# Optimization experiments

Measured on AMD Instinct MI355X. Metric: run time of the kernel, lower is better.

The kernel has to match this reference:

```python
import jax, jax.numpy as jnp
import numpy as np

B_SI = 4.1491   # neutron scattering length Si (fm)
B_O = 5.803     # neutron scattering length O (fm)
CUTOFF = 3.5    # tetrahedral neighbour cutoff (A)
BIG = 1e6       # masked-distance sentinel (finite to keep grads NaN-free)


def setup_inputs() -> dict:
    key = jax.random.key(0)
    k1, k2 = jax.random.split(key)
    N, L = 4096, 40.0
    positions = jax.random.uniform(k1, (N, 3), dtype=jnp.float32) * L
    cell = (L * jnp.eye(3)).astype(jnp.float32)
    r_bins = (0.05 + 0.05 * jnp.arange(200, dtype=jnp.float32))      # 0.05..10.0 A
    q_bins = jnp.linspace(0.5, 25.0, 500, dtype=jnp.float32)          # A^-1
    species = jax.random.randint(k2, (N,), 0, 3, dtype=jnp.int32)     # 0=Si, 1/2=O
    return {"positions": positions, "cell": cell, "r_bins": r_bins,
            "q_bins": q_bins, "species": species}


def _pair_geometry(positions, cell):
    # Minimum-image displacements under a general periodic cell.
    disp = positions[:, None, :] - positions[None, :, :]        # [N,N,3]
    frac = disp @ jnp.linalg.inv(cell)
    frac = frac - jnp.round(frac)
    disp = frac @ cell
    d2 = jnp.sum(disp * disp, axis=-1)                           # [N,N]
    self_mask = jnp.eye(positions.shape[0], dtype=bool)
    dist = jnp.sqrt(jnp.where(self_mask, 1.0, d2))               # safe sqrt on diag
    return disp, dist, self_mask


def reference(positions, cell, r_bins, q_bins, species):
    N = positions.shape[0]
    nbins = r_bins.shape[0]
    dtype = positions.dtype

    disp, dist, self_mask = _pair_geometry(positions, cell)

    # --- neutron-weighted G(r): differentiable linear (cloud-in-cell) binning ---
    b = jnp.where(species == 0, B_SI, B_O).astype(dtype)         # per-atom scattering length
    w = (b[:, None] * b[None, :]) / (jnp.mean(b) ** 2)           # Faber-Ziman pair weights
    r0, dr = r_bins[0], r_bins[1] - r_bins[0]
    x = (dist - r0) / dr
    i0 = jnp.floor(x).astype(jnp.int32)
    f = x - i0.astype(dtype)
    valid = (~self_mask) & (i0 >= 0) & (i0 < nbins - 1)
    w0 = jnp.where(valid, w * (1.0 - f), 0.0).ravel()
    w1 = jnp.where(valid, w * f, 0.0).ravel()
    i0f = jnp.clip(i0, 0, nbins - 1).ravel()
    hist = (jnp.zeros(nbins, dtype)
            .at[i0f].add(w0)
            .at[jnp.clip(i0f + 1, 0, nbins - 1)].add(w1))
    V = jnp.abs(jnp.linalg.det(cell))
    rho = N / V
    shell = 4.0 * jnp.pi * r_bins ** 2 * dr                       # ideal-gas shell volume
    G_r = hist / (N * rho * shell)                                # [nbins]

    # --- total correlation function T(r) = 4 pi rho r G(r) ---
    T_r = 4.0 * jnp.pi * rho * r_bins * G_r

    # --- structure factor S(Q) = 1 + 4 pi rho int r^2 (G(r)-1) sinc(Qr) dr ---
    qr = q_bins[:, None] * r_bins[None, :]                        # [nQ, nr]
    integrand = (r_bins ** 2) * (G_r - 1.0)
    S_Q = 1.0 + 4.0 * jnp.pi * rho * dr * jnp.sum(
        integrand[None, :] * jnp.sinc(qr / jnp.pi), axis=1)

    # --- tetrahedral order parameter q_tet over Si centres with O neighbours ---
    central = species == 0
    nbr_ok = (species != 0)[None, :] & (~self_mask)
    nd = jnp.where(nbr_ok, dist, BIG)
    negd, idx = jax.lax.top_k(-nd, 4)                             # 4 nearest O per atom
    d4 = -negd                                                    # [N,4]
    u = jnp.take_along_axis(disp, idx[:, :, None], axis=1) / d4[:, :, None]  # unit vecs
    cosang = jnp.einsum('nkd,nld->nkl', u, u)                     # [N,4,4]
    pair_mask = jnp.triu(jnp.ones((4, 4), bool), 1)               # 6 angle pairs
    q_i = 1.0 - (3.0 / 8.0) * jnp.sum(((cosang + 1.0 / 3.0) ** 2) * pair_mask, axis=(1, 2))
    vf = (central & (d4[:, 3] < CUTOFF)).astype(dtype)            # needs 4 nbrs in cutoff
    q_tet = jnp.sum(q_i * vf) / jnp.maximum(jnp.sum(vf), 1.0)

    return G_r, T_r, S_Q, q_tet
```

## Files before the change

### kernel.cpp

```cpp
#include <hip/hip_runtime.h>
#include <climits>
#include <math.h>


#define B_SI_F 4.1491f
#define B_O_F  5.803f
#define CUTOFF_F 3.5f
#define CS2 12.25350025f
#define NCOPIES 16
#define CAP 32

#define WS_HIST 16
#define WS_ACC  3328
#define WS_CNT  4096

__device__ __forceinline__ bool dless(float da, int ia, float db, int ib) {
    return (da < db) || (da == db && ia < ib);
}

struct CellK {
    float ci0, ci1, ci2, ci3, ci4, ci5, ci6, ci7, ci8;
    float c0, c1, c2, c3, c4, c5, c6, c7, c8;
};

__device__ __forceinline__ CellK make_cell(const float* __restrict__ cellm,
                                           bool& diag) {
    CellK K;
    K.c0 = cellm[0]; K.c1 = cellm[1]; K.c2 = cellm[2];
    K.c3 = cellm[3]; K.c4 = cellm[4]; K.c5 = cellm[5];
    K.c6 = cellm[6]; K.c7 = cellm[7]; K.c8 = cellm[8];
    double m0 = K.c0, m1 = K.c1, m2 = K.c2;
    double m3 = K.c3, m4 = K.c4, m5 = K.c5;
    double m6 = K.c6, m7 = K.c7, m8 = K.c8;
    double det = m0*(m4*m8 - m5*m7) - m1*(m3*m8 - m5*m6) + m2*(m3*m7 - m4*m6);
    double rd = 1.0 / det;
    K.ci0 = (float)( (m4*m8 - m5*m7) * rd);
    K.ci1 = (float)(-(m1*m8 - m2*m7) * rd);
    K.ci2 = (float)( (m1*m5 - m2*m4) * rd);
    K.ci3 = (float)(-(m3*m8 - m5*m6) * rd);
    K.ci4 = (float)( (m0*m8 - m2*m6) * rd);
    K.ci5 = (float)(-(m0*m5 - m2*m3) * rd);
    K.ci6 = (float)( (m3*m7 - m4*m6) * rd);
    K.ci7 = (float)(-(m0*m7 - m1*m6) * rd);
    K.ci8 = (float)( (m0*m4 - m1*m3) * rd);
    diag = (K.c1 == 0.0f) && (K.c2 == 0.0f) && (K.c3 == 0.0f) &&
           (K.c5 == 0.0f) && (K.c6 == 0.0f) && (K.c7 == 0.0f);
    return K;
}

template<bool DIAG>
__device__ __forceinline__ void min_image(const CellK& K,
                                          float dx, float dy, float dz,
                                          float& ex, float& ey, float& ez) {
    if (DIAG) {
        float t0 = dx * K.ci0, t1 = dy * K.ci4, t2 = dz * K.ci8;
        t0 -= rintf(t0);  t1 -= rintf(t1);  t2 -= rintf(t2);
        ex = t0 * K.c0;  ey = t1 * K.c4;  ez = t2 * K.c8;
    } else {
        float f0 = dx*K.ci0 + dy*K.ci3 + dz*K.ci6;
        float f1 = dx*K.ci1 + dy*K.ci4 + dz*K.ci7;
        float f2 = dx*K.ci2 + dy*K.ci5 + dz*K.ci8;
        f0 -= rintf(f0);  f1 -= rintf(f1);  f2 -= rintf(f2);
        ex = f0*K.c0 + f1*K.c3 + f2*K.c6;
        ey = f0*K.c1 + f1*K.c4 + f2*K.c7;
        ez = f0*K.c2 + f1*K.c5 + f2*K.c8;
    }
}

template<bool DIAG>
__device__ __forceinline__ void hist_sweep(const CellK& K,
                                           const float4* __restrict__ sj,
                                           const float4* __restrict__ sjc,
                                           int lbase, int jb0,
                                           float fi0, float fi1, float fi2,
                                           float xi, float yi, float zi,
                                           float wi, float inv_dr, float nrb0,
                                           float dmax2, int nbins_m1,
                                           float* shist,
                                           bool iSi, bool iO, bool offdiag, int iidx,
                                           float* __restrict__ cnt,
                                           float4* __restrict__ cand) {
    #pragma unroll 4
    for (int l = 0; l < 32; ++l) {
        const float4 pj = sj[lbase + l];
        float d0 = fi0 - pj.x;  d0 -= rintf(d0);
        float d1 = fi1 - pj.y;  d1 -= rintf(d1);
        float d2 = fi2 - pj.z;  d2 -= rintf(d2);
        float ex, ey, ez;
        if (DIAG) {
            ex = d0 * K.c0;  ey = d1 * K.c4;  ez = d2 * K.c8;
        } else {
            ex = d0*K.c0 + d1*K.c3 + d2*K.c6;
            ey = d0*K.c1 + d1*K.c4 + d2*K.c7;
            ez = d0*K.c2 + d1*K.c5 + d2*K.c8;
        }
        float dsq = fmaf(ex, ex, fmaf(ey, ey, ez * ez));
        if (dsq < dmax2) {
            float dist = __builtin_amdgcn_sqrtf(dsq);
            float x  = fmaf(dist, inv_dr, nrb0);
            float fl = floorf(x);
            int   i0 = (int)fl;
            if ((unsigned)i0 < (unsigned)nbins_m1) {
                float w  = wi * pj.w;
                float wf = w * (x - fl);
                atomicAdd(&shist[i0],     w - wf);
                atomicAdd(&shist[i0 + 1], wf);
            }
            if (dsq < CS2) {
                const int jg = jb0 + lbase + l;
                if (iSi && pj.w == B_O_F) {
                    float old = atomicAdd(&cnt[iidx], 1.0f);
                    int slot = (int)rintf(old);
                    if (slot < CAP) {
                        float4 cj = sjc[lbase + l];
                        cj.w = __int_as_float(jg);
                        cand[iidx * CAP + slot] = cj;
                    }
                }
                if (offdiag && iO && pj.w == B_SI_F) {
                    float old = atomicAdd(&cnt[jg], 1.0f);
                    int slot = (int)rintf(old);
                    if (slot < CAP)
                        cand[jg * CAP + slot] = make_float4(xi, yi, zi, __int_as_float(iidx));
                }
            }
        }
    }
}

__global__ __launch_bounds__(256) void k_main(const float* __restrict__ cellm,
                                              const float* __restrict__ pos,
                                              const int* __restrict__ species,
                                              const float* __restrict__ rbins,
                                              float* __restrict__ ws,
                                              int N, int nbins, int T) {
    const int tid = threadIdx.x;
    const int bid = blockIdx.x;

    bool diag;
    const CellK K = make_cell(cellm, diag);

    __shared__ float shist[256];
    __shared__ float sjf[64 * 4];
    __shared__ float sjc[64 * 4];
    shist[tid] = 0.0f;

    const int jhalf = bid & 1;
    int rem = bid >> 1, ti = 0;
    while (rem >= T - ti) { rem -= T - ti; ti++; }
    const int tj  = ti + rem;
    const int jb0 = tj * 128 + jhalf * 64;

    if (tid < 192) {
        int g = 3 * jb0 + tid;
        sjc[(tid / 3) * 4 + (tid % 3)] = (g < 3 * N) ? pos[g] : 0.0f;
    } else {
        int a = tid - 192;
        int ja = jb0 + a;
        sjf[a * 4 + 3] = (ja < N) ? ((species[ja] == 0) ? B_SI_F : B_O_F) : 0.0f;
    }
    __syncthreads();
    if (tid < 64) {
        float x = sjc[tid*4], y = sjc[tid*4+1], z = sjc[tid*4+2];
        float f0, f1, f2;
        if (diag) { f0 = x*K.ci0; f1 = y*K.ci4; f2 = z*K.ci8; }
        else {
            f0 = x*K.ci0 + y*K.ci3 + z*K.ci6;
            f1 = x*K.ci1 + y*K.ci4 + z*K.ci7;
            f2 = x*K.ci2 + y*K.ci5 + z*K.ci8;
        }
        sjf[tid*4] = f0;  sjf[tid*4+1] = f1;  sjf[tid*4+2] = f2;
    }

    const float rb0      = rbins[0];
    const float dr       = rbins[1] - rbins[0];
    const float inv_dr   = 1.0f / dr;
    const float nrb0     = -rb0 * inv_dr;
    const int   nbins_m1 = nbins - 1;
    const float dmax     = fmaf((float)nbins_m1, dr, rb0);
    const float dmax2    = dmax * dmax * 1.000001f;

    const int il  = tid & 127;
    const int sub = tid >> 7;
    const int i   = ti * 128 + il;
    const int ig  = min(i, N - 1);
    const float xi = pos[3*ig], yi = pos[3*ig+1], zi = pos[3*ig+2];
    float fi0, fi1, fi2;
    if (diag) { fi0 = xi*K.ci0; fi1 = yi*K.ci4; fi2 = zi*K.ci8; }
    else {
        fi0 = xi*K.ci0 + yi*K.ci3 + zi*K.ci6;
        fi1 = xi*K.ci1 + yi*K.ci4 + zi*K.ci7;
        fi2 = xi*K.ci2 + yi*K.ci5 + zi*K.ci8;
    }
    const int   spi  = species[ig];
    const float b_i  = (spi == 0) ? B_SI_F : B_O_F;
    const float wmul = (ti == tj) ? 1.0f : 2.0f;
    const float wi   = (i < N) ? b_i * wmul : 0.0f;
    const bool iSi = (i < N) && (spi == 0);
    const bool iO  = (i < N) && (spi != 0);
    const bool offdiag = (ti != tj);

    float*  cnt  = ws + WS_CNT;
    float4* cand = (float4*)(ws + WS_CNT + (size_t)N);

    __syncthreads();

    const float4* sj   = (const float4*)sjf;
    const float4* sjc4 = (const float4*)sjc;
    const int lbase = sub * 32;
    if (diag) hist_sweep<true >(K, sj, sjc4, lbase, jb0, fi0, fi1, fi2, xi, yi, zi, wi, inv_dr, nrb0, dmax2, nbins_m1, shist, iSi, iO, offdiag, i, cnt, cand);
    else      hist_sweep<false>(K, sj, sjc4, lbase, jb0, fi0, fi1, fi2, xi, yi, zi, wi, inv_dr, nrb0, dmax2, nbins_m1, shist, iSi, iO, offdiag, i, cnt, cand);

    __syncthreads();

    float* gh = ws + WS_HIST + (size_t)(bid % NCOPIES) * nbins;
    for (int t = tid; t < nbins; t += 256) {
        float h = shist[t];
        if (h != 0.0f) atomicAdd(&gh[t], h);
    }
}

#define INS4D(c, jc, ex, ey, ez)                                           \
{                                                                          \
    if (dless(c, jc, e3, j3)) {                                            \
        bool lt2 = dless(c, jc, e2, j2);                                   \
        bool lt1 = dless(c, jc, e1, j1);                                   \
        bool lt0 = dless(c, jc, e0, j0);                                   \
        e3 = lt2 ? e2 : c;               j3 = lt2 ? j2 : jc;               \
        x3 = lt2 ? x2 : ex;  y3 = lt2 ? y2 : ey;  z3 = lt2 ? z2 : ez;      \
        e2 = lt2 ? (lt1 ? e1 : c) : e2;  j2 = lt2 ? (lt1 ? j1 : jc) : j2;  \
        x2 = lt2 ? (lt1 ? x1 : ex) : x2;                                   \
        y2 = lt2 ? (lt1 ? y1 : ey) : y2;                                   \
        z2 = lt2 ? (lt1 ? z1 : ez) : z2;                                   \
        e1 = lt1 ? (lt0 ? e0 : c) : e1;  j1 = lt1 ? (lt0 ? j0 : jc) : j1;  \
        x1 = lt1 ? (lt0 ? x0 : ex) : x1;                                   \
        y1 = lt1 ? (lt0 ? y0 : ey) : y1;                                   \
        z1 = lt1 ? (lt0 ? z0 : ez) : z1;                                   \
        e0 = lt0 ? c : e0;               j0 = lt0 ? jc : j0;               \
        x0 = lt0 ? ex : x0;  y0 = lt0 ? ey : y0;  z0 = lt0 ? ez : z0;      \
    }                                                                      \
}

__device__ __forceinline__ float fast_sinc(float x) {
    float rev = x * 0.15915494309189535f;
    rev -= rintf(rev);
    float sn = __builtin_amdgcn_sinf(rev);
    return sn * __builtin_amdgcn_rcpf(x);
}

__global__ __launch_bounds__(256) void k_fin(const float* __restrict__ cellm,
                                             float* __restrict__ ws,
                                             const float* __restrict__ rbins,
                                             const float* __restrict__ qbins,
                                             const int* __restrict__ species,
                                             const float* __restrict__ pos,
                                             float* __restrict__ out,
                                             int N, int nbins, int nq,
                                             int QB, int BT) {
    const int tid = threadIdx.x;
    const int bid = blockIdx.x;

    if (bid >= QB) {
        __shared__ float swq[4], swv[4];
        __shared__ float sacc[128];
        __shared__ int   slast;
        const int tb   = bid - QB;
        const int wid  = tid >> 6;
        const int lane = tid & 63;
        const int s = __builtin_amdgcn_readfirstlane(tb * 4 + wid);

        float* cnt = ws + WS_CNT;
        const float4* cand = (const float4*)(ws + WS_CNT + (size_t)N);

        float qiv = 0.0f, vf = 0.0f;
        if (s < N && species[s] == 0) {
            bool diag;
            const CellK K = make_cell(cellm, diag);
            const float xi = pos[3*s], yi = pos[3*s+1], zi = pos[3*s+2];
            const int c = (int)rintf(cnt[s]);
            if (lane == 0) cnt[s] = 0.0f;

            float e0 = 1e30f, e1 = 1e30f, e2 = 1e30f, e3 = 1e30f;
            int   j0 = INT_MAX, j1 = INT_MAX, j2 = INT_MAX, j3 = INT_MAX;
            float x0 = 0, y0 = 0, z0 = 0, x1 = 0, y1 = 0, z1 = 0;
            float x2 = 0, y2 = 0, z2 = 0, x3 = 0, y3 = 0, z3 = 0;

            if (c <= CAP) {
                if (lane < c) {
                    float4 cd = cand[s * CAP + lane];
                    int j = __float_as_int(cd.w);
                    float ex, ey, ez;
                    if (diag) min_image<true >(K, xi - cd.x, yi - cd.y, zi - cd.z, ex, ey, ez);
                    else      min_image<false>(K, xi - cd.x, yi - cd.y, zi - cd.z, ex, ey, ez);
                    e0 = fmaf(ex, ex, fmaf(ey, ey, ez * ez));
                    j0 = j;  x0 = ex;  y0 = ey;  z0 = ez;
                }
            } else {
                for (int k = lane; k < N; k += 64) {
                    int   sp = species[k];
                    float px = pos[3*k], py = pos[3*k+1], pz = pos[3*k+2];
                    float ex, ey, ez;
                    if (diag) min_image<true >(K, xi - px, yi - py, zi - pz, ex, ey, ez);
                    else      min_image<false>(K, xi - px, yi - py, zi - pz, ex, ey, ez);
                    float d2 = fmaf(ex, ex, fmaf(ey, ey, ez * ez));
                    float cc = (sp != 0 && k != s) ? d2 : 1e30f;
                    int   jc = k;
                    INS4D(cc, jc, ex, ey, ez)
                }
            }

            float r0d, r1d, r2d, r3d;
            int   r0j, r1j, r2j, r3j;
            float rx[4], ry[4], rz[4];
            #define EXTRACT_MIN(RD, RJ, RK)                                    \
            {                                                                  \
                float md = e0; int mj = j0;                                    \
                float mx = x0, my = y0, mz = z0;                               \
                for (int off = 32; off > 0; off >>= 1) {                       \
                    float od = __shfl_xor(md, off, 64);                        \
                    int   oj = __shfl_xor(mj, off, 64);                        \
                    float ox = __shfl_xor(mx, off, 64);                        \
                    float oy = __shfl_xor(my, off, 64);                        \
                    float oz = __shfl_xor(mz, off, 64);                        \
                    bool keep = dless(md, mj, od, oj);                         \
                    md = keep ? md : od;  mj = keep ? mj : oj;                 \
                    mx = keep ? mx : ox;  my = keep ? my : oy;                 \
                    mz = keep ? mz : oz;                                       \
                }                                                              \
                RD = md; RJ = mj; rx[RK] = mx; ry[RK] = my; rz[RK] = mz;       \
                bool pop = (j0 == mj);                                         \
                e0 = pop ? e1 : e0;  j0 = pop ? j1 : j0;                       \
                x0 = pop ? x1 : x0;  y0 = pop ? y1 : y0;  z0 = pop ? z1 : z0;  \
                e1 = pop ? e2 : e1;  j1 = pop ? j2 : j1;                       \
                x1 = pop ? x2 : x1;  y1 = pop ? y2 : y1;  z1 = pop ? z2 : z1;  \
                e2 = pop ? e3 : e2;  j2 = pop ? j3 : j2;                       \
                x2 = pop ? x3 : x2;  y2 = pop ? y3 : y2;  z2 = pop ? z3 : z2;  \
                e3 = pop ? 1e30f : e3;  j3 = pop ? INT_MAX : j3;               \
            }
            EXTRACT_MIN(r0d, r0j, 0)
            EXTRACT_MIN(r1d, r1j, 1)
            EXTRACT_MIN(r2d, r2j, 2)
            EXTRACT_MIN(r3d, r3j, 3)
            #undef EXTRACT_MIN

            if (lane == 0 && r3j != INT_MAX) {
                float dd[4] = {sqrtf(r0d), sqrtf(r1d), sqrtf(r2d), sqrtf(r3d)};
                if (dd[3] < CUTOFF_F) {
                    float ux[4], uy[4], uz[4];
                    #pragma unroll
                    for (int k = 0; k < 4; ++k) {
                        ux[k] = rx[k] / dd[k];
                        uy[k] = ry[k] / dd[k];
                        uz[k] = rz[k] / dd[k];
                    }
                    float s2 = 0.0f;
                    #pragma unroll
                    for (int k = 0; k < 4; ++k)
                        #pragma unroll
                        for (int l = k + 1; l < 4; ++l) {
                            float cs = ux[k]*ux[l] + uy[k]*uy[l] + uz[k]*uz[l];
                            float t  = cs + (1.0f / 3.0f);
                            s2 += t * t;
                        }
                    qiv = 1.0f - 0.375f * s2;
                    vf  = 1.0f;
                }
            }
        }
        if (lane == 0) { swq[wid] = qiv; swv[wid] = vf; }
        __syncthreads();
        if (tid == 0) {
            float bsq = swq[0] + swq[1] + swq[2] + swq[3];
            float bsv = swv[0] + swv[1] + swv[2] + swv[3];
            atomicAdd(&ws[WS_ACC + (tb & 63)], bsq);
            atomicAdd(&ws[WS_ACC + 64 + (tb & 63)], bsv);
            asm volatile("s_waitcnt vmcnt(0)" ::: "memory");
            float old = atomicAdd(&ws[WS_ACC + 128], 1.0f);
            slast = (old > (float)BT - 1.5f) ? 1 : 0;
        }
        __syncthreads();
        if (slast) {
            if (tid < 128) sacc[tid] = atomicAdd(&ws[WS_ACC + tid], 0.0f);
            __syncthreads();
            if (tid == 0) {
                float tq = 0.0f, tv = 0.0f;
                for (int k = 0; k < 64; ++k) { tq += sacc[k]; tv += sacc[64 + k]; }
                out[2 * nbins + nq] = tq / fmaxf(tv, 1.0f);
            }
        }
        return;
    }

    __shared__ float2 srw[256];
    __shared__ int    scnt[256];

    double m0 = cellm[0], m1 = cellm[1], m2 = cellm[2];
    double m3 = cellm[3], m4 = cellm[4], m5 = cellm[5];
    double m6 = cellm[6], m7 = cellm[7], m8 = cellm[8];
    double det = m0*(m4*m8 - m5*m7) - m1*(m3*m8 - m5*m6) + m2*(m3*m7 - m4*m6);
    const float rho = (float)((double)N / fabs(det));

    {
        int c = 0;
        for (int k = tid; k < N; k += 256) c += (species[k] == 0) ? 1 : 0;
        scnt[tid] = c;
    }
    __syncthreads();
    for (int s = 128; s > 0; s >>= 1) {
        if (tid < s) scnt[tid] += scnt[tid + s];
        __syncthreads();
    }
    const int nSi = scnt[0];
    const float mean_b  = ((float)nSi * B_SI_F + (float)(N - nSi) * B_O_F) / (float)N;
    const float w_scale = 1.0f / (mean_b * mean_b);

    const float dr = rbins[1] - rbins[0];
    const float FOURPI = 4.0f * 3.14159265358979323846f;

    for (int t = tid; t < nbins; t += blockDim.x) {
        float h = 0.0f;
        #pragma unroll
        for (int c = 0; c < NCOPIES; ++c) h += ws[WS_HIST + c * nbins + t];
        h *= w_scale;
        float r = rbins[t];
        float shell = FOURPI * r * r * dr;
        float g = h / ((float)N * rho * shell);
        srw[t] = make_float2(r, r * r * (g - 1.0f));
        if (bid == 0) {
            out[t] = g;
            out[nbins + t] = FOURPI * rho * r * g;
        }
    }
    __syncthreads();

    int q = bid * blockDim.x + tid;
    if (q < nq) {
        float qq = qbins[q];
        float s0 = 0.0f, s1 = 0.0f, s2 = 0.0f, s3 = 0.0f;
        int t = 0;
        for (; t + 4 <= nbins; t += 4) {
            float2 a = srw[t], b = srw[t+1], c = srw[t+2], d = srw[t+3];
            s0 += a.y * fast_sinc(qq * a.x);
            s1 += b.y * fast_sinc(qq * b.x);
            s2 += c.y * fast_sinc(qq * c.x);
            s3 += d.y * fast_sinc(qq * d.x);
        }
        for (; t < nbins; ++t) {
            float2 a = srw[t];
            s0 += a.y * fast_sinc(qq * a.x);
        }
        float s = (s0 + s1) + (s2 + s3);
        out[2 * nbins + q] = 1.0f + FOURPI * rho * dr * s;
    }
}

extern "C" void kernel_launch(void* const* d_in, const int* in_sizes, int n_in,
                              void* d_out, int out_size, void* d_ws, size_t ws_size,
                              hipStream_t stream) {
    const float* pos     = (const float*)d_in[0];
    const float* cell    = (const float*)d_in[1];
    const float* rbins   = (const float*)d_in[2];
    const float* qbins   = (const float*)d_in[3];
    const int*   species = (const int*)d_in[4];
    float* out = (float*)d_out;
    float* ws  = (float*)d_ws;

    const int N     = in_sizes[4];
    const int nbins = in_sizes[2];
    const int nq    = in_sizes[3];

    const int T  = (N + 127) / 128;
    const int P2 = T * (T + 1);
    const int BT = (N + 3) / 4;
    const int QB = (nq + 255) / 256;

    k_main<<<P2, 256, 0, stream>>>(cell, pos, species, rbins, ws, N, nbins, T);
    k_fin<<<QB + BT, 256, 0, stream>>>(cell, ws, rbins, qbins, species, pos, out, N, nbins, nq, QB, BT);
}
```

Before: 93.83 us.

## Fuse histogram and finish kernels with a device-wide atomic barrier

```diff
diff --git a/kernel.cpp b/kernel.cpp
--- a/kernel.cpp
+++ b/kernel.cpp
@@ -12,6 +12,8 @@
 
 #define WS_HIST 16
 #define WS_ACC  3328
+#define WS_TDONE (WS_ACC + 128)
+#define WS_HDONE (WS_ACC + 129)
 #define WS_CNT  4096
 
 __device__ __forceinline__ bool dless(float da, int ia, float db, int ib) {
@@ -67,6 +69,18 @@
     }
 }
 
+union U64F2 { unsigned long long u; float2 f; };
+
+__device__ __forceinline__ void cand_store(float* cand_base, size_t slot_idx,
+                                           float cx, float cy, float cz, int jg) {
+    unsigned long long* cp = (unsigned long long*)(cand_base + slot_idx * 4);
+    U64F2 a, b;
+    a.f = make_float2(cx, cy);
+    b.f = make_float2(cz, __int_as_float(jg));
+    atomicExch(cp,     a.u);
+    atomicExch(cp + 1, b.u);
+}
+
 template<bool DIAG>
 __device__ __forceinline__ void hist_sweep(const CellK& K,
                                            const float4* __restrict__ sj,
@@ -79,7 +93,7 @@
                                            float* shist,
                                            bool iSi, bool iO, bool offdiag, int iidx,
                                            float* __restrict__ cnt,
-                                           float4* __restrict__ cand) {
+                                           float* __restrict__ cand) {
     #pragma unroll 4
     for (int l = 0; l < 32; ++l) {
         const float4 pj = sj[lbase + l];
@@ -113,30 +127,27 @@
                     int slot = (int)rintf(old);
                     if (slot < CAP) {
                         float4 cj = sjc[lbase + l];
-                        cj.w = __int_as_float(jg);
-                        cand[iidx * CAP + slot] = cj;
+                        cand_store(cand, (size_t)iidx * CAP + slot, cj.x, cj.y, cj.z, jg);
                     }
                 }
                 if (offdiag && iO && pj.w == B_SI_F) {
                     float old = atomicAdd(&cnt[jg], 1.0f);
                     int slot = (int)rintf(old);
                     if (slot < CAP)
-                        cand[jg * CAP + slot] = make_float4(xi, yi, zi, __int_as_float(iidx));
+                        cand_store(cand, (size_t)jg * CAP + slot, xi, yi, zi, iidx);
                 }
             }
         }
     }
 }
 
-__global__ __launch_bounds__(256) void k_main(const float* __restrict__ cellm,
-                                              const float* __restrict__ pos,
-                                              const int* __restrict__ species,
-                                              const float* __restrict__ rbins,
-                                              float* __restrict__ ws,
-                                              int N, int nbins, int T) {
-    const int tid = threadIdx.x;
-    const int bid = blockIdx.x;
-
+__device__ __forceinline__ void hist_block(int bid, int tid,
+                                           const float* __restrict__ cellm,
+                                           const float* __restrict__ pos,
+                                           const int* __restrict__ species,
+                                           const float* __restrict__ rbins,
+                                           float* __restrict__ ws,
+                                           int N, int nbins, int T) {
     bool diag;
     const CellK K = make_cell(cellm, diag);
 
@@ -200,8 +211,8 @@
     const bool iO  = (i < N) && (spi != 0);
     const bool offdiag = (ti != tj);
 
-    float*  cnt  = ws + WS_CNT;
-    float4* cand = (float4*)(ws + WS_CNT + (size_t)N);
+    float* cnt  = ws + WS_CNT;
+    float* cand = ws + WS_CNT + (size_t)N;
 
     __syncthreads();
 
@@ -248,18 +259,16 @@
     return sn * __builtin_amdgcn_rcpf(x);
 }
 
-__global__ __launch_bounds__(256) void k_fin(const float* __restrict__ cellm,
-                                             float* __restrict__ ws,
-                                             const float* __restrict__ rbins,
-                                             const float* __restrict__ qbins,
-                                             const int* __restrict__ species,
-                                             const float* __restrict__ pos,
-                                             float* __restrict__ out,
-                                             int N, int nbins, int nq,
-                                             int QB, int BT) {
-    const int tid = threadIdx.x;
-    const int bid = blockIdx.x;
-
+__device__ __forceinline__ void fin_block(int bid, int tid,
+                                          const float* __restrict__ cellm,
+                                          float* __restrict__ ws,
+                                          const float* __restrict__ rbins,
+                                          const float* __restrict__ qbins,
+                                          const int* __restrict__ species,
+                                          const float* __restrict__ pos,
+                                          float* __restrict__ out,
+                                          int N, int nbins, int nq,
+                                          int QB, int BT) {
     if (bid >= QB) {
         __shared__ float swq[4], swv[4];
         __shared__ float sacc[128];
@@ -269,16 +278,21 @@
         const int lane = tid & 63;
         const int s = __builtin_amdgcn_readfirstlane(tb * 4 + wid);
 
-        float* cnt = ws + WS_CNT;
-        const float4* cand = (const float4*)(ws + WS_CNT + (size_t)N);
+        float* cnt  = ws + WS_CNT;
+        float* cand = ws + WS_CNT + (size_t)N;
 
         float qiv = 0.0f, vf = 0.0f;
         if (s < N && species[s] == 0) {
             bool diag;
             const CellK K = make_cell(cellm, diag);
             const float xi = pos[3*s], yi = pos[3*s+1], zi = pos[3*s+2];
-            const int c = (int)rintf(cnt[s]);
-            if (lane == 0) cnt[s] = 0.0f;
+            float cf = 0.0f;
+            if (lane == 0) {
+                cf = atomicAdd(&cnt[s], 0.0f);
+                atomicExch(&cnt[s], 0.0f);
+            }
+            cf = __shfl(cf, 0, 64);
+            const int c = (int)rintf(cf);
 
             float e0 = 1e30f, e1 = 1e30f, e2 = 1e30f, e3 = 1e30f;
             int   j0 = INT_MAX, j1 = INT_MAX, j2 = INT_MAX, j3 = INT_MAX;
@@ -287,11 +301,15 @@
 
             if (c <= CAP) {
                 if (lane < c) {
-                    float4 cd = cand[s * CAP + lane];
-                    int j = __float_as_int(cd.w);
+                    unsigned long long* cp =
+                        (unsigned long long*)(cand + ((size_t)s * CAP + lane) * 4);
+                    U64F2 a, b;
+                    a.u = atomicAdd(cp,     0ULL);
+                    b.u = atomicAdd(cp + 1, 0ULL);
+                    int j = __float_as_int(b.f.y);
                     float ex, ey, ez;
-                    if (diag) min_image<true >(K, xi - cd.x, yi - cd.y, zi - cd.z, ex, ey, ez);
-                    else      min_image<false>(K, xi - cd.x, yi - cd.y, zi - cd.z, ex, ey, ez);
+                    if (diag) min_image<true >(K, xi - a.f.x, yi - a.f.y, zi - b.f.x, ex, ey, ez);
+                    else      min_image<false>(K, xi - a.f.x, yi - a.f.y, zi - b.f.x, ex, ey, ez);
                     e0 = fmaf(ex, ex, fmaf(ey, ey, ez * ez));
                     j0 = j;  x0 = ex;  y0 = ey;  z0 = ez;
                 }
@@ -375,7 +393,7 @@
             atomicAdd(&ws[WS_ACC + (tb & 63)], bsq);
             atomicAdd(&ws[WS_ACC + 64 + (tb & 63)], bsv);
             asm volatile("s_waitcnt vmcnt(0)" ::: "memory");
-            float old = atomicAdd(&ws[WS_ACC + 128], 1.0f);
+            float old = atomicAdd(&ws[WS_TDONE], 1.0f);
             slast = (old > (float)BT - 1.5f) ? 1 : 0;
         }
         __syncthreads();
@@ -417,10 +435,11 @@
     const float dr = rbins[1] - rbins[0];
     const float FOURPI = 4.0f * 3.14159265358979323846f;
 
-    for (int t = tid; t < nbins; t += blockDim.x) {
+    for (int t = tid; t < nbins; t += 256) {
         float h = 0.0f;
         #pragma unroll
-        for (int c = 0; c < NCOPIES; ++c) h += ws[WS_HIST + c * nbins + t];
+        for (int c = 0; c < NCOPIES; ++c)
+            h += atomicAdd(&ws[WS_HIST + c * nbins + t], 0.0f);
         h *= w_scale;
         float r = rbins[t];
         float shell = FOURPI * r * r * dr;
@@ -433,7 +452,7 @@
     }
     __syncthreads();
 
-    int q = bid * blockDim.x + tid;
+    int q = bid * 256 + tid;
     if (q < nq) {
         float qq = qbins[q];
         float s0 = 0.0f, s1 = 0.0f, s2 = 0.0f, s3 = 0.0f;
@@ -454,6 +473,62 @@
     }
 }
 
+__global__ __launch_bounds__(256, 5)
+void k_fused(const float* __restrict__ cellm,
+             const float* __restrict__ pos,
+             const int* __restrict__ species,
+             const float* __restrict__ rbins,
+             const float* __restrict__ qbins,
+             float* __restrict__ ws,
+             float* __restrict__ out,
+             int N, int nbins, int nq, int T, int P2, int QB, int BT) {
+    const int bid = blockIdx.x;
+    const int tid = threadIdx.x;
+
+    hist_block(bid, tid, cellm, pos, species, rbins, ws, N, nbins, T);
+
+    __syncthreads();
+    if (tid == 0) {
+        asm volatile("s_waitcnt vmcnt(0)" ::: "memory");
+        atomicAdd(&ws[WS_HDONE], 1.0f);
+    }
+
+    if (bid < QB + BT) {
+        __shared__ int sgo;
+        if (tid == 0) {
+            while (atomicAdd(&ws[WS_HDONE], 0.0f) < (float)P2)
+                __builtin_amdgcn_s_sleep(2);
+            sgo = 1;
+        }
+        __syncthreads();
+        (void)sgo;
+        fin_block(bid, tid, cellm, ws, rbins, qbins, species, pos, out,
+                  N, nbins, nq, QB, BT);
+    }
+}
+
+__global__ __launch_bounds__(256)
+void k_main_sep(const float* __restrict__ cellm,
+                const float* __restrict__ pos,
+                const int* __restrict__ species,
+                const float* __restrict__ rbins,
+                float* __restrict__ ws, int N, int nbins, int T) {
+    hist_block(blockIdx.x, threadIdx.x, cellm, pos, species, rbins, ws, N, nbins, T);
+}
+
+__global__ __launch_bounds__(256)
+void k_fin_sep(const float* __restrict__ cellm,
+               float* __restrict__ ws,
+               const float* __restrict__ rbins,
+               const float* __restrict__ qbins,
+               const int* __restrict__ species,
+               const float* __restrict__ pos,
+               float* __restrict__ out,
+               int N, int nbins, int nq, int QB, int BT) {
+    fin_block(blockIdx.x, threadIdx.x, cellm, ws, rbins, qbins, species, pos, out,
+              N, nbins, nq, QB, BT);
+}
+
 extern "C" void kernel_launch(void* const* d_in, const int* in_sizes, int n_in,
                               void* d_out, int out_size, void* d_ws, size_t ws_size,
                               hipStream_t stream) {
@@ -474,6 +549,14 @@
     const int BT = (N + 3) / 4;
     const int QB = (nq + 255) / 256;
 
-    k_main<<<P2, 256, 0, stream>>>(cell, pos, species, rbins, ws, N, nbins, T);
-    k_fin<<<QB + BT, 256, 0, stream>>>(cell, ws, rbins, qbins, species, pos, out, N, nbins, nq, QB, BT);
-}
+    const bool fused_ok = (P2 >= QB + BT) && (P2 <= 1280);
+
+    if (fused_ok) {
+        k_fused<<<P2, 256, 0, stream>>>(cell, pos, species, rbins, qbins,
+                                        ws, out, N, nbins, nq, T, P2, QB, BT);
+    } else {
+        k_main_sep<<<P2, 256, 0, stream>>>(cell, pos, species, rbins, ws, N, nbins, T);
+        k_fin_sep<<<QB + BT, 256, 0, stream>>>(cell, ws, rbins, qbins, species, pos,
+                                               out, N, nbins, nq, QB, BT);
+    }
+}
```

After: 184.7 us. +96.8%, slower.
